# Kernel optimization log

Hardware: AMD Instinct MI355X
Metric: run time of the kernel (lower is better)

The kernel has to match this reference:

```python
import jax, jax.numpy as jnp
import numpy as np

K_RATIO = 0.2
EPS = 1e-6


def setup_inputs() -> dict:
    key = jax.random.key(0)
    k1, k2 = jax.random.split(key)
    B, C, D, H, W = 2, 4, 128, 128, 128
    logits = jax.random.normal(k1, (B, C, D, H, W), dtype=jnp.float32)
    labels = jax.random.randint(k2, (B, D, H, W), 0, C)
    # one-hot target along channel axis 1, matching the tensor-path `target` arg
    target = jax.nn.one_hot(labels, C, axis=1, dtype=jnp.float32)
    return {"logits": logits, "target": target}


def reference(logits, target):
    B, C = logits.shape[0], logits.shape[1]

    # ---- Top-K cross entropy (ignore_index=-1 -> all voxels valid) ----
    y = jnp.argmax(target, axis=1)  # [B, D, H, W] int labels
    logp = jax.nn.log_softmax(logits, axis=1)
    # CE per voxel: -logp[b, y, d, h, w]
    ce = -jnp.take_along_axis(logp, y[:, None], axis=1)[:, 0]  # [B, D, H, W]
    ce_flat = ce.reshape(B, -1)  # [B, N]
    N = ce_flat.shape[1]
    k = max(1, int(N * K_RATIO))  # static: all voxels valid, k < N
    topk_vals, _ = jax.lax.top_k(ce_flat, k)  # [B, k]
    topk_loss = jnp.mean(jnp.mean(topk_vals, axis=1))

    # ---- Soft dice (no valid_mask in tensor path) ----
    p = jax.nn.softmax(logits, axis=1)  # [B, C, D, H, W]
    spatial = tuple(range(2, p.ndim))
    num = 2.0 * jnp.sum(p * target, axis=spatial)          # [B, C]
    den = jnp.sum(p + target, axis=spatial) + EPS          # [B, C]
    dice = 1.0 - num / den                                  # [B, C]
    if C > 1:
        dice = dice[:, 1:]  # drop background channel
    dice_loss = jnp.mean(dice)

    return topk_loss + 0.5 * dice_loss
```

## Files before the change

### kernel.cpp

```cpp
#include <hip/hip_runtime.h>
#include <stdint.h>

#define NVOX (1u << 21)
#define NB   2
#define KSEL 419430u
#define TPB  256
#define VPB  4096
#define BPB  ((int)(NVOX / VPB))
#define NBLK (NB * BPB)
#define NCOPY 64
#define NHC  16
#define NBIN2 8192
#define SH2  18

__device__ __forceinline__ float wred64(float v) {
#pragma unroll
  for (int o = 32; o > 0; o >>= 1) v += __shfl_down(v, o, 64);
  return v;
}

__global__ __launch_bounds__(TPB, 2) void k1_fused(
    const float* __restrict__ logits, const float* __restrict__ target,
    uint32_t* __restrict__ hcnt, float* __restrict__ hsum,
    float* __restrict__ dice_acc )
{
  __shared__ uint32_t scnt[NBIN2];
  __shared__ float    ssum[NBIN2];
  const int tid = threadIdx.x;
  for (int i = tid; i < NBIN2; i += TPB) { scnt[i] = 0; ssum[i] = 0.f; }
  __syncthreads();

  const int blk = blockIdx.x;
  const int b = blk / BPB;
  const size_t v0 = (size_t)(blk % BPB) * VPB;
  const float* lg = logits + (size_t)b * 4 * NVOX + v0;
  const float* tg = target + (size_t)b * 4 * NVOX + v0;

  float sp[4] = {0.f,0.f,0.f,0.f}, nm[4] = {0.f,0.f,0.f,0.f}, ct[4] = {0.f,0.f,0.f,0.f};

  for (int i = tid * 4; i < VPB; i += TPB * 4) {
    float4 L[4], T[4];
#pragma unroll
    for (int c = 0; c < 4; ++c) {
      L[c] = *(const float4*)(lg + (size_t)c * NVOX + i);
      T[c] = *(const float4*)(tg + (size_t)c * NVOX + i);
    }
#pragma unroll
    for (int j = 0; j < 4; ++j) {
      float l[4], t[4];
#pragma unroll
      for (int c = 0; c < 4; ++c) {
        l[c] = ((const float*)&L[c])[j];
        t[c] = ((const float*)&T[c])[j];
      }
      float m = fmaxf(fmaxf(l[0], l[1]), fmaxf(l[2], l[3]));
      float e[4]; float s = 0.f;
#pragma unroll
      for (int c = 0; c < 4; ++c) { e[c] = __expf(l[c] - m); s += e[c]; }
      float inv = 1.f / s;
      float lse = __logf(s);
      float ly = l[0]*t[0] + l[1]*t[1] + l[2]*t[2] + l[3]*t[3];
      float cev = (m - ly) + lse;
      uint32_t idx = __float_as_uint(cev) >> SH2;
      if (idx >= NBIN2) idx = NBIN2 - 1;
      atomicAdd(&scnt[idx], 1u);
      atomicAdd(&ssum[idx], cev);
#pragma unroll
      for (int c = 0; c < 4; ++c) {
        float p = e[c] * inv;
        sp[c] += p;
        nm[c] += p * t[c];
        ct[c] += t[c];
      }
    }
  }

#pragma unroll
  for (int c = 0; c < 4; ++c) { sp[c] = wred64(sp[c]); nm[c] = wred64(nm[c]); ct[c] = wred64(ct[c]); }
  if ((tid & 63) == 0) {
    float* dst = dice_acc + ((size_t)(blk & (NCOPY - 1)) * NB + b) * 12;
#pragma unroll
    for (int c = 0; c < 4; ++c) {
      atomicAdd(dst + c,     sp[c]);
      atomicAdd(dst + 4 + c, nm[c]);
      atomicAdd(dst + 8 + c, ct[c]);
    }
  }
  __syncthreads();
  const size_t hoff = ((size_t)b * NHC + (size_t)(blk & (NHC - 1))) * NBIN2;
  uint32_t* cdst = hcnt + hoff;
  float*    sdst = hsum + hoff;
  for (int i = tid; i < NBIN2; i += TPB) {
    uint32_t cv = scnt[i];
    if (cv) {
      atomicAdd(&cdst[i], cv);
      atomicAdd(&sdst[i], ssum[i]);
    }
  }
}

__global__ __launch_bounds__(256) void k_reduce(
    const uint32_t* __restrict__ hcnt, const float* __restrict__ hsum,
    uint32_t* __restrict__ rcnt, float* __restrict__ rsum)
{
  const int b = blockIdx.x >> 3;
  const int seg = blockIdx.x & 7;
  const int base = seg * 1024 + threadIdx.x * 4;
  uint4 c = {0,0,0,0};
  float4 s = {0.f,0.f,0.f,0.f};
  for (int copy = 0; copy < NHC; ++copy) {
    const size_t off = ((size_t)b * NHC + copy) * NBIN2 + base;
    uint4 cv = *(const uint4*)(hcnt + off);
    float4 sv = *(const float4*)(hsum + off);
    c.x += cv.x; c.y += cv.y; c.z += cv.z; c.w += cv.w;
    s.x += sv.x; s.y += sv.y; s.z += sv.z; s.w += sv.w;
  }
  *(uint4*)(rcnt + (size_t)b * NBIN2 + base) = c;
  *(float4*)(rsum + (size_t)b * NBIN2 + base) = s;
}

__global__ __launch_bounds__(256) void k_final(
    const uint32_t* __restrict__ rcnt, const float* __restrict__ rsum,
    const float* __restrict__ dice_acc, float* __restrict__ out)
{
  __shared__ uint32_t shc[NBIN2];
  __shared__ uint32_t chunk[256];
  __shared__ uint32_t sbkt, srem;
  __shared__ float wpart[4];
  __shared__ float ts[NB];
  __shared__ float comp[24];
  const int tid = threadIdx.x;

  for (int b = 0; b < NB; ++b) {
    const uint32_t* rc = rcnt + (size_t)b * NBIN2;
    const float*    rs = rsum + (size_t)b * NBIN2;
    uint32_t s = 0;
    for (int j = 0; j < 32; ++j) {
      uint32_t v = rc[tid * 32 + j];
      shc[tid * 32 + j] = v;
      s += v;
    }
    chunk[tid] = s;
    __syncthreads();
    if (tid == 0) {
      uint32_t k = KSEL, cum = 0;
      int ci = 255;
      for (; ci > 0; --ci) {
        uint32_t c = chunk[ci];
        if (cum + c >= k) break;
        cum += c;
      }
      int bkt = ci * 32;
      for (int j = 31; j >= 0; --j) {
        uint32_t c = shc[ci * 32 + j];
        if (cum + c >= k) { bkt = ci * 32 + j; break; }
        cum += c;
      }
      sbkt = (uint32_t)bkt;
      srem = k - cum;
    }
    __syncthreads();
    const int bkt = (int)sbkt;
    float w = 0.f;
    for (int j = 0; j < 32; ++j) {
      int bin = tid * 32 + j;
      if (bin > bkt) w += rs[bin];
    }
    w = wred64(w);
    if ((tid & 63) == 0) wpart[tid >> 6] = w;
    __syncthreads();
    if (tid == 0) {
      float cnt_t = (float)shc[bkt];
      float sum_t = rs[bkt];
      float lo = __uint_as_float((uint32_t)bkt << SH2);
      float hi = __uint_as_float((uint32_t)(bkt + 1) << SH2);
      float width = hi - lo;
      float avg = sum_t / cnt_t;
      float frac = (float)srem / cnt_t;
      float est = avg + (1.f - frac) * 0.5f * width;
      ts[b] = wpart[0] + wpart[1] + wpart[2] + wpart[3] + (float)srem * est;
    }
    __syncthreads();
  }

  if (tid < 24) {
    float a = 0.f;
    for (int r = 0; r < NCOPY; ++r) a += dice_acc[(size_t)r * 24 + tid];
    comp[tid] = a;
  }
  __syncthreads();
  if (tid == 0) {
    float dl = 0.f;
#pragma unroll
    for (int b = 0; b < 2; ++b)
#pragma unroll
      for (int c = 1; c < 4; ++c) {
        float sp = comp[b * 12 + c];
        float nm = comp[b * 12 + 4 + c];
        float ct = comp[b * 12 + 8 + c];
        dl += 1.f - (2.f * nm) / (sp + ct + 1e-6f);
      }
    float topk = 0.5f * (ts[0] + ts[1]) / (float)KSEL;
    out[0] = topk + 0.5f * (dl / 6.f);
  }
}

extern "C" void kernel_launch(void* const* d_in, const int* in_sizes, int n_in,
                              void* d_out, int out_size, void* d_ws, size_t ws_size,
                              hipStream_t stream) {
  (void)in_sizes; (void)n_in; (void)out_size; (void)ws_size;
  const float* logits = (const float*)d_in[0];
  const float* target = (const float*)d_in[1];
  float* out = (float*)d_out;

  char* ws = (char*)d_ws;
  uint32_t* hcnt = (uint32_t*)ws;
  float*    hsum = (float*)(hcnt + (size_t)NB * NHC * NBIN2);
  float*    dice_acc = hsum + (size_t)NB * NHC * NBIN2;
  uint32_t* rcnt = (uint32_t*)(dice_acc + (size_t)NCOPY * NB * 12);
  float*    rsum = (float*)(rcnt + (size_t)NB * NBIN2);
  const size_t ZERO_BYTES = (size_t)((char*)(dice_acc + (size_t)NCOPY * NB * 12) - ws);

  hipMemsetAsync(hcnt, 0, ZERO_BYTES, stream);

  k1_fused<<<NBLK, TPB, 0, stream>>>(logits, target, hcnt, hsum, dice_acc);
  k_reduce<<<NB * 8, 256, 0, stream>>>(hcnt, hsum, rcnt, rsum);
  k_final<<<1, 256, 0, stream>>>(rcnt, rsum, dice_acc, out);
}
```

Before: 191.2 us.

## Pack histogram count and fixed-point sum into single 64-bit LDS atomic

The per-block shared histogram is halved to 4096 bins with a coarser float-bit shift. Count and a fixed-point scaled CE sum are packed into one 64-bit word, so each voxel does one LDS atomic instead of two (including a float atomic). Shared memory drops from 64KB to 32KB, and launch bounds rise to 4 blocks per CU for more occupancy. The downstream reduce and final kernels are resized to match. The cost is coarser bins, which makes the top-k tail interpolation less accurate, and fixed-point rounding in the per-bin sums.

```diff
diff --git a/kernel.cpp b/kernel.cpp
--- a/kernel.cpp
+++ b/kernel.cpp
@@ -10,8 +10,9 @@
 #define NBLK (NB * BPB)
 #define NCOPY 64
 #define NHC  16
-#define NBIN2 8192
-#define SH2  18
+#define NBINS 4096
+#define SH   19
+#define FIXS 262144.0f
 
 __device__ __forceinline__ float wred64(float v) {
 #pragma unroll
@@ -19,15 +20,14 @@
   return v;
 }
 
-__global__ __launch_bounds__(TPB, 2) void k1_fused(
+__global__ __launch_bounds__(TPB, 4) void k1_fused(
     const float* __restrict__ logits, const float* __restrict__ target,
     uint32_t* __restrict__ hcnt, float* __restrict__ hsum,
     float* __restrict__ dice_acc )
 {
-  __shared__ uint32_t scnt[NBIN2];
-  __shared__ float    ssum[NBIN2];
+  __shared__ unsigned long long hbin[NBINS];
   const int tid = threadIdx.x;
-  for (int i = tid; i < NBIN2; i += TPB) { scnt[i] = 0; ssum[i] = 0.f; }
+  for (int i = tid; i < NBINS; i += TPB) hbin[i] = 0ull;
   __syncthreads();
 
   const int blk = blockIdx.x;
@@ -61,10 +61,10 @@
       float lse = __logf(s);
       float ly = l[0]*t[0] + l[1]*t[1] + l[2]*t[2] + l[3]*t[3];
       float cev = (m - ly) + lse;
-      uint32_t idx = __float_as_uint(cev) >> SH2;
-      if (idx >= NBIN2) idx = NBIN2 - 1;
-      atomicAdd(&scnt[idx], 1u);
-      atomicAdd(&ssum[idx], cev);
+      uint32_t idx = __float_as_uint(cev) >> SH;
+      if (idx > NBINS - 1) idx = NBINS - 1;
+      unsigned long long pk = (1ull << 40) | (unsigned long long)(cev * FIXS);
+      atomicAdd(&hbin[idx], pk);
 #pragma unroll
       for (int c = 0; c < 4; ++c) {
         float p = e[c] * inv;
@@ -87,14 +87,14 @@
     }
   }
   __syncthreads();
-  const size_t hoff = ((size_t)b * NHC + (size_t)(blk & (NHC - 1))) * NBIN2;
+  const size_t hoff = ((size_t)b * NHC + (size_t)(blk & (NHC - 1))) * NBINS;
   uint32_t* cdst = hcnt + hoff;
   float*    sdst = hsum + hoff;
-  for (int i = tid; i < NBIN2; i += TPB) {
-    uint32_t cv = scnt[i];
-    if (cv) {
-      atomicAdd(&cdst[i], cv);
-      atomicAdd(&sdst[i], ssum[i]);
+  for (int i = tid; i < NBINS; i += TPB) {
+    unsigned long long v = hbin[i];
+    if (v) {
+      atomicAdd(&cdst[i], (uint32_t)(v >> 40));
+      atomicAdd(&sdst[i], (float)(v & 0xFFFFFFFFFFull) * (1.0f / FIXS));
     }
   }
 }
@@ -103,27 +103,27 @@
     const uint32_t* __restrict__ hcnt, const float* __restrict__ hsum,
     uint32_t* __restrict__ rcnt, float* __restrict__ rsum)
 {
-  const int b = blockIdx.x >> 3;
-  const int seg = blockIdx.x & 7;
+  const int b = blockIdx.x >> 2;
+  const int seg = blockIdx.x & 3;
   const int base = seg * 1024 + threadIdx.x * 4;
   uint4 c = {0,0,0,0};
   float4 s = {0.f,0.f,0.f,0.f};
   for (int copy = 0; copy < NHC; ++copy) {
-    const size_t off = ((size_t)b * NHC + copy) * NBIN2 + base;
+    const size_t off = ((size_t)b * NHC + copy) * NBINS + base;
     uint4 cv = *(const uint4*)(hcnt + off);
     float4 sv = *(const float4*)(hsum + off);
     c.x += cv.x; c.y += cv.y; c.z += cv.z; c.w += cv.w;
     s.x += sv.x; s.y += sv.y; s.z += sv.z; s.w += sv.w;
   }
-  *(uint4*)(rcnt + (size_t)b * NBIN2 + base) = c;
-  *(float4*)(rsum + (size_t)b * NBIN2 + base) = s;
+  *(uint4*)(rcnt + (size_t)b * NBINS + base) = c;
+  *(float4*)(rsum + (size_t)b * NBINS + base) = s;
 }
 
 __global__ __launch_bounds__(256) void k_final(
     const uint32_t* __restrict__ rcnt, const float* __restrict__ rsum,
     const float* __restrict__ dice_acc, float* __restrict__ out)
 {
-  __shared__ uint32_t shc[NBIN2];
+  __shared__ uint32_t shc[NBINS];
   __shared__ uint32_t chunk[256];
   __shared__ uint32_t sbkt, srem;
   __shared__ float wpart[4];
@@ -132,13 +132,14 @@
   const int tid = threadIdx.x;
 
   for (int b = 0; b < NB; ++b) {
-    const uint32_t* rc = rcnt + (size_t)b * NBIN2;
-    const float*    rs = rsum + (size_t)b * NBIN2;
+    const uint32_t* rc = rcnt + (size_t)b * NBINS;
+    const float*    rs = rsum + (size_t)b * NBINS;
     uint32_t s = 0;
-    for (int j = 0; j < 32; ++j) {
-      uint32_t v = rc[tid * 32 + j];
-      shc[tid * 32 + j] = v;
-      s += v;
+#pragma unroll
+    for (int q = 0; q < 4; ++q) {
+      uint4 v = *(const uint4*)(rc + tid * 16 + q * 4);
+      *(uint4*)&shc[tid * 16 + q * 4] = v;
+      s += v.x + v.y + v.z + v.w;
     }
     chunk[tid] = s;
     __syncthreads();
@@ -150,10 +151,10 @@
         if (cum + c >= k) break;
         cum += c;
       }
-      int bkt = ci * 32;
-      for (int j = 31; j >= 0; --j) {
-        uint32_t c = shc[ci * 32 + j];
-        if (cum + c >= k) { bkt = ci * 32 + j; break; }
+      int bkt = ci * 16;
+      for (int j = 15; j >= 0; --j) {
+        uint32_t c = shc[ci * 16 + j];
+        if (cum + c >= k) { bkt = ci * 16 + j; break; }
         cum += c;
       }
       sbkt = (uint32_t)bkt;
@@ -162,8 +163,9 @@
     __syncthreads();
     const int bkt = (int)sbkt;
     float w = 0.f;
-    for (int j = 0; j < 32; ++j) {
-      int bin = tid * 32 + j;
+#pragma unroll
+    for (int j = 0; j < 16; ++j) {
+      int bin = tid * 16 + j;
       if (bin > bkt) w += rs[bin];
     }
     w = wred64(w);
@@ -172,8 +174,8 @@
     if (tid == 0) {
       float cnt_t = (float)shc[bkt];
       float sum_t = rs[bkt];
-      float lo = __uint_as_float((uint32_t)bkt << SH2);
-      float hi = __uint_as_float((uint32_t)(bkt + 1) << SH2);
+      float lo = __uint_as_float((uint32_t)bkt << SH);
+      float hi = __uint_as_float((uint32_t)(bkt + 1) << SH);
       float width = hi - lo;
       float avg = sum_t / cnt_t;
       float frac = (float)srem / cnt_t;
@@ -215,15 +217,15 @@
 
   char* ws = (char*)d_ws;
   uint32_t* hcnt = (uint32_t*)ws;
-  float*    hsum = (float*)(hcnt + (size_t)NB * NHC * NBIN2);
-  float*    dice_acc = hsum + (size_t)NB * NHC * NBIN2;
+  float*    hsum = (float*)(hcnt + (size_t)NB * NHC * NBINS);
+  float*    dice_acc = hsum + (size_t)NB * NHC * NBINS;
   uint32_t* rcnt = (uint32_t*)(dice_acc + (size_t)NCOPY * NB * 12);
-  float*    rsum = (float*)(rcnt + (size_t)NB * NBIN2);
+  float*    rsum = (float*)(rcnt + (size_t)NB * NBINS);
   const size_t ZERO_BYTES = (size_t)((char*)(dice_acc + (size_t)NCOPY * NB * 12) - ws);
 
   hipMemsetAsync(hcnt, 0, ZERO_BYTES, stream);
 
   k1_fused<<<NBLK, TPB, 0, stream>>>(logits, target, hcnt, hsum, dice_acc);
-  k_reduce<<<NB * 8, 256, 0, stream>>>(hcnt, hsum, rcnt, rsum);
+  k_reduce<<<NB * 4, 256, 0, stream>>>(hcnt, hsum, rcnt, rsum);
   k_final<<<1, 256, 0, stream>>>(rcnt, rsum, dice_acc, out);
 }
```

Measured after the change: 176.4 us. -7.8%, faster.
